# Performance work log

Hardware: AMD Instinct MI355X
Metric: run time of the kernel (lower is better)

The kernel has to match this reference:

```python
import jax, jax.numpy as jnp
import numpy as np

SELF_IMPORTANCE = 0.25  # blend weight for the node's own transformed features


def setup_inputs() -> dict:
    key = jax.random.key(0)
    k1, k2, k3, k4, k5 = jax.random.split(key, 5)
    F, newF, N = 128, 64, 500000
    return {
        "x": jax.random.normal(k1, (1, F), dtype=jnp.float32),
        "X": jax.random.normal(k2, (N, F), dtype=jnp.float32),
        "kernel": jax.random.normal(k3, (F, newF), dtype=jnp.float32) * (1.0 / np.sqrt(F)),
        "attn_self": jax.random.normal(k4, (newF, 1), dtype=jnp.float32) * (1.0 / np.sqrt(newF)),
        "attn_neigh": jax.random.normal(k5, (newF, 1), dtype=jnp.float32) * (1.0 / np.sqrt(newF)),
    }


def reference(x, X, kernel, attn_self, attn_neigh):
    # x: [1, F] node features; X: [N, F] neighbor features
    x_t = x @ kernel            # [1, newF]
    X_t = X @ kernel            # [N, newF]
    a_self = x_t @ attn_self    # [1, 1]
    a_neigh = X_t @ attn_neigh  # [N, 1]
    # repeat_elements(a_self, N) + a_neigh, then transpose -> [1, N]
    scores = (a_self + a_neigh).T
    # original adds mask = exp(-1e10) * -1e10 == -0.0 (a no-op); faithful softmax:
    attn = jax.nn.softmax(scores, axis=-1)  # [1, N]
    # Dropout is identity at inference (eval mode)
    feats_neigh = attn @ X_t    # [1, newF]
    return (1.0 - SELF_IMPORTANCE) * feats_neigh + SELF_IMPORTANCE * x_t
```

## Files before the change

kernel.cpp:

```cpp
#include <hip/hip_runtime.h>
#include <math.h>


#define TPB 256
#define MAXBLK 2048
#define PART_STRIDE 136
#define PART_BASE 256
#define FIN_TPB 512

__global__ __launch_bounds__(128) void gat_prep(
    const float* __restrict__ x, const float* __restrict__ kern,
    const float* __restrict__ attn_neigh, float* __restrict__ ws) {
  int t = threadIdx.x;
  float s = 0.f;
#pragma unroll 8
  for (int c = 0; c < 64; ++c) s += kern[t * 64 + c] * attn_neigh[c];
  ws[t] = s;
  if (t < 64) {
    float s2 = 0.f;
#pragma unroll 8
    for (int j = 0; j < 128; ++j) s2 += x[j] * kern[j * 64 + t];
    ws[128 + t] = s2;
  }
}

__global__ __launch_bounds__(TPB, 8) void gat_main(
    const float4* __restrict__ X4, const float* __restrict__ ws,
    float* __restrict__ part, int N, int totalWaves) {
  const int lane = threadIdx.x & 63;
  const int half = lane >> 5;
  const int hl = lane & 31;
  const int wid = threadIdx.x >> 6;
  const int gwave = blockIdx.x * (TPB / 64) + wid;

  const float4 wv = ((const float4*)ws)[hl];

  const int npairs = N >> 1;
  const int stride = totalWaves;

  float m = -INFINITY, l = 0.f;
  float ax = 0.f, ay = 0.f, az = 0.f, aw = 0.f;

  int p = gwave;
  float4 xv = make_float4(0.f, 0.f, 0.f, 0.f);
  if (p < npairs) xv = X4[(size_t)p * 64 + lane];

  for (; p + stride < npairs; p += stride) {
    const float4 xn = X4[(size_t)(p + stride) * 64 + lane];

    float s = xv.x * wv.x + xv.y * wv.y + xv.z * wv.z + xv.w * wv.w;
    s += __shfl_xor(s, 1);  s += __shfl_xor(s, 2);  s += __shfl_xor(s, 4);
    s += __shfl_xor(s, 8);  s += __shfl_xor(s, 16);
    const float mn = fmaxf(m, s);
    const float corr = __expf(m - mn);
    const float pw = __expf(s - mn);
    l = l * corr + pw;
    ax = ax * corr + pw * xv.x;  ay = ay * corr + pw * xv.y;
    az = az * corr + pw * xv.z;  aw = aw * corr + pw * xv.w;
    m = mn;

    xv = xn;
  }
  if (p < npairs) {
    float s = xv.x * wv.x + xv.y * wv.y + xv.z * wv.z + xv.w * wv.w;
    s += __shfl_xor(s, 1);  s += __shfl_xor(s, 2);  s += __shfl_xor(s, 4);
    s += __shfl_xor(s, 8);  s += __shfl_xor(s, 16);
    const float mn = fmaxf(m, s);
    const float corr = __expf(m - mn);
    const float pw = __expf(s - mn);
    l = l * corr + pw;
    ax = ax * corr + pw * xv.x;  ay = ay * corr + pw * xv.y;
    az = az * corr + pw * xv.z;  aw = aw * corr + pw * xv.w;
    m = mn;
  }

  if ((N & 1) && gwave == 0) {
    float4 tv = make_float4(0.f, 0.f, 0.f, 0.f);
    if (half == 0) tv = X4[(size_t)(N - 1) * 32 + hl];
    float s = tv.x * wv.x + tv.y * wv.y + tv.z * wv.z + tv.w * wv.w;
    s += __shfl_xor(s, 1);  s += __shfl_xor(s, 2);  s += __shfl_xor(s, 4);
    s += __shfl_xor(s, 8);  s += __shfl_xor(s, 16);
    if (half == 0) {
      const float mn = fmaxf(m, s);
      const float corr = __expf(m - mn);
      const float pw = __expf(s - mn);
      l = l * corr + pw;
      ax = ax * corr + pw * tv.x;  ay = ay * corr + pw * tv.y;
      az = az * corr + pw * tv.z;  aw = aw * corr + pw * tv.w;
      m = mn;
    }
  }

  const float m_o = __shfl_xor(m, 32);
  const float l_o = __shfl_xor(l, 32);
  const float axo = __shfl_xor(ax, 32);
  const float ayo = __shfl_xor(ay, 32);
  const float azo = __shfl_xor(az, 32);
  const float awo = __shfl_xor(aw, 32);
  const float M2 = fmaxf(m, m_o);
  const float c0 = (m == -INFINITY) ? 0.f : __expf(m - M2);
  const float c1 = (m_o == -INFINITY) ? 0.f : __expf(m_o - M2);
  const float l2 = l * c0 + l_o * c1;
  const float bx = ax * c0 + axo * c1;
  const float by = ay * c0 + ayo * c1;
  const float bz = az * c0 + azo * c1;
  const float bw = aw * c0 + awo * c1;

  __shared__ float sm[TPB / 64];
  __shared__ float sl[TPB / 64];
  __shared__ float sacc[TPB / 64][128];
  if (lane < 32) {
    sacc[wid][hl * 4 + 0] = bx;
    sacc[wid][hl * 4 + 1] = by;
    sacc[wid][hl * 4 + 2] = bz;
    sacc[wid][hl * 4 + 3] = bw;
    if (hl == 0) { sm[wid] = M2; sl[wid] = l2; }
  }
  __syncthreads();

  if (threadIdx.x < 32) {
    float Mb = -INFINITY;
#pragma unroll
    for (int w2 = 0; w2 < TPB / 64; ++w2) Mb = fmaxf(Mb, sm[w2]);
    float Lb = 0.f, fx = 0.f, fy = 0.f, fz = 0.f, fw = 0.f;
#pragma unroll
    for (int w2 = 0; w2 < TPB / 64; ++w2) {
      const float sc = (sm[w2] == -INFINITY) ? 0.f : __expf(sm[w2] - Mb);
      Lb += sc * sl[w2];
      fx += sc * sacc[w2][hl * 4 + 0];
      fy += sc * sacc[w2][hl * 4 + 1];
      fz += sc * sacc[w2][hl * 4 + 2];
      fw += sc * sacc[w2][hl * 4 + 3];
    }
    float* pb = part + (size_t)blockIdx.x * PART_STRIDE;
    if (hl == 0) { pb[0] = Mb; pb[1] = Lb; }
    float4 v = make_float4(fx, fy, fz, fw);
    ((float4*)(pb + 8))[hl] = v;
  }
}

__global__ __launch_bounds__(FIN_TPB) void gat_fin(
    const float* __restrict__ kern, const float* __restrict__ ws,
    float* __restrict__ out, int nblk) {
  __shared__ float scale[MAXBLK];
  __shared__ float red[FIN_TPB];
  __shared__ float fpart[4][128];
  __shared__ float feats[128];
  const int t = threadIdx.x;
  const float* part = ws + PART_BASE;

  float m = -INFINITY;
  for (int b = t; b < nblk; b += FIN_TPB) m = fmaxf(m, part[(size_t)b * PART_STRIDE]);
  red[t] = m;
  __syncthreads();
  for (int s = FIN_TPB / 2; s > 0; s >>= 1) {
    if (t < s) red[t] = fmaxf(red[t], red[t + s]);
    __syncthreads();
  }
  const float M = red[0];
  __syncthreads();

  float lp = 0.f;
  for (int b = t; b < nblk; b += FIN_TPB) {
    const float mb = part[(size_t)b * PART_STRIDE];
    const float sc = (mb == -INFINITY) ? 0.f : __expf(mb - M);
    scale[b] = sc;
    lp += sc * part[(size_t)b * PART_STRIDE + 1];
  }
  red[t] = lp;
  __syncthreads();
  for (int s = FIN_TPB / 2; s > 0; s >>= 1) {
    if (t < s) red[t] += red[t + s];
    __syncthreads();
  }
  const float L = red[0];
  __syncthreads();

  {
    const int j = t & 127;
    const int q = t >> 7;
    float f = 0.f;
    for (int b = q; b < nblk; b += 4) f += scale[b] * part[(size_t)b * PART_STRIDE + 8 + j];
    fpart[q][j] = f;
  }
  __syncthreads();
  if (t < 128) feats[t] = (fpart[0][t] + fpart[1][t] + fpart[2][t] + fpart[3][t]) / L;
  __syncthreads();

  if (t < 64) {
    float s = 0.f;
#pragma unroll 8
    for (int j = 0; j < 128; ++j) s += feats[j] * kern[j * 64 + t];
    out[t] = 0.75f * s + 0.25f * ws[128 + t];
  }
}

extern "C" void kernel_launch(void* const* d_in, const int* in_sizes, int n_in,
                              void* d_out, int out_size, void* d_ws, size_t ws_size,
                              hipStream_t stream) {
  const float* x          = (const float*)d_in[0];
  const float* X          = (const float*)d_in[1];
  const float* kern       = (const float*)d_in[2];
  const float* attn_neigh = (const float*)d_in[4];
  float* ws  = (float*)d_ws;
  float* out = (float*)d_out;

  const int N = in_sizes[1] / 128;

  int nblk = MAXBLK;
  const size_t availF = ws_size / 4;
  if (availF < (size_t)PART_BASE + (size_t)MAXBLK * PART_STRIDE) {
    long cap = ((long)availF - PART_BASE) / PART_STRIDE;
    nblk = (cap < 1) ? 1 : (int)cap;
  }
  const int totalWaves = nblk * (TPB / 64);

  gat_prep<<<1, 128, 0, stream>>>(x, kern, attn_neigh, ws);
  gat_main<<<nblk, TPB, 0, stream>>>((const float4*)X, ws, ws + PART_BASE,
                                     N, totalWaves);
  gat_fin<<<1, FIN_TPB, 0, stream>>>(kern, ws, out, nblk);
}
```

Measured before the change: 484.6 us.

## Deepen X prefetch, use fewer larger blocks, store partials column-major

The main kernel now keeps two rows of X loaded ahead instead of one. It launches 512 blocks of 512 threads instead of 2048 blocks of 256, which halves the total number of waves. Per-block softmax partials are stored column-major, so the final kernel reads them with unit stride and reduces each feature with wave shuffles. The aim is to keep memory-level parallelism with fewer blocks and to cheapen the finalize pass, at the risk of lower occupancy on a bandwidth-bound stream.

```diff
diff --git a/kernel.cpp b/kernel.cpp
--- a/kernel.cpp
+++ b/kernel.cpp
@@ -2,9 +2,8 @@
 #include <math.h>
 
 
-#define TPB 256
-#define MAXBLK 2048
-#define PART_STRIDE 136
+#define TPB 512
+#define NBLK 512
 #define PART_BASE 256
 #define FIN_TPB 512
 
@@ -24,55 +23,50 @@
   }
 }
 
-__global__ __launch_bounds__(TPB, 8) void gat_main(
+__global__ __launch_bounds__(TPB, 4) void gat_main(
     const float4* __restrict__ X4, const float* __restrict__ ws,
-    float* __restrict__ part, int N, int totalWaves) {
+    float* __restrict__ part, int N, int nblk) {
   const int lane = threadIdx.x & 63;
   const int half = lane >> 5;
   const int hl = lane & 31;
   const int wid = threadIdx.x >> 6;
   const int gwave = blockIdx.x * (TPB / 64) + wid;
+  const int stride = nblk * (TPB / 64);
 
   const float4 wv = ((const float4*)ws)[hl];
 
   const int npairs = N >> 1;
-  const int stride = totalWaves;
 
   float m = -INFINITY, l = 0.f;
   float ax = 0.f, ay = 0.f, az = 0.f, aw = 0.f;
 
+#define PROC(XV)                                                            \
+  {                                                                         \
+    float s = (XV).x * wv.x + (XV).y * wv.y + (XV).z * wv.z + (XV).w * wv.w;\
+    s += __shfl_xor(s, 1);  s += __shfl_xor(s, 2);  s += __shfl_xor(s, 4);  \
+    s += __shfl_xor(s, 8);  s += __shfl_xor(s, 16);                         \
+    const float mn = fmaxf(m, s);                                           \
+    const float corr = __expf(m - mn);               \
+    const float pw = __expf(s - mn);                                        \
+    l = l * corr + pw;                                                      \
+    ax = ax * corr + pw * (XV).x;  ay = ay * corr + pw * (XV).y;            \
+    az = az * corr + pw * (XV).z;  aw = aw * corr + pw * (XV).w;            \
+    m = mn;                                                                 \
+  }
+
   int p = gwave;
-  float4 xv = make_float4(0.f, 0.f, 0.f, 0.f);
-  if (p < npairs) xv = X4[(size_t)p * 64 + lane];
-
-  for (; p + stride < npairs; p += stride) {
-    const float4 xn = X4[(size_t)(p + stride) * 64 + lane];
-
-    float s = xv.x * wv.x + xv.y * wv.y + xv.z * wv.z + xv.w * wv.w;
-    s += __shfl_xor(s, 1);  s += __shfl_xor(s, 2);  s += __shfl_xor(s, 4);
-    s += __shfl_xor(s, 8);  s += __shfl_xor(s, 16);
-    const float mn = fmaxf(m, s);
-    const float corr = __expf(m - mn);
-    const float pw = __expf(s - mn);
-    l = l * corr + pw;
-    ax = ax * corr + pw * xv.x;  ay = ay * corr + pw * xv.y;
-    az = az * corr + pw * xv.z;  aw = aw * corr + pw * xv.w;
-    m = mn;
-
-    xv = xn;
-  }
-  if (p < npairs) {
-    float s = xv.x * wv.x + xv.y * wv.y + xv.z * wv.z + xv.w * wv.w;
-    s += __shfl_xor(s, 1);  s += __shfl_xor(s, 2);  s += __shfl_xor(s, 4);
-    s += __shfl_xor(s, 8);  s += __shfl_xor(s, 16);
-    const float mn = fmaxf(m, s);
-    const float corr = __expf(m - mn);
-    const float pw = __expf(s - mn);
-    l = l * corr + pw;
-    ax = ax * corr + pw * xv.x;  ay = ay * corr + pw * xv.y;
-    az = az * corr + pw * xv.z;  aw = aw * corr + pw * xv.w;
-    m = mn;
-  }
+  float4 x0 = make_float4(0.f, 0.f, 0.f, 0.f);
+  float4 x1 = make_float4(0.f, 0.f, 0.f, 0.f);
+  if (p < npairs) x0 = X4[(size_t)p * 64 + lane];
+  if (p + stride < npairs) x1 = X4[(size_t)(p + stride) * 64 + lane];
+  for (; p + 2 * stride < npairs; p += stride) {
+    const float4 xn = X4[(size_t)(p + 2 * stride) * 64 + lane];
+    PROC(x0);
+    x0 = x1;
+    x1 = xn;
+  }
+  if (p < npairs) PROC(x0);
+  if (p + stride < npairs) PROC(x1);
 
   if ((N & 1) && gwave == 0) {
     float4 tv = make_float4(0.f, 0.f, 0.f, 0.f);
@@ -90,6 +84,7 @@
       m = mn;
     }
   }
+#undef PROC
 
   const float m_o = __shfl_xor(m, 32);
   const float l_o = __shfl_xor(l, 32);
@@ -132,25 +127,33 @@
       fz += sc * sacc[w2][hl * 4 + 2];
       fw += sc * sacc[w2][hl * 4 + 3];
     }
-    float* pb = part + (size_t)blockIdx.x * PART_STRIDE;
-    if (hl == 0) { pb[0] = Mb; pb[1] = Lb; }
-    float4 v = make_float4(fx, fy, fz, fw);
-    ((float4*)(pb + 8))[hl] = v;
+    const int b = blockIdx.x;
+    float* part_m = part;
+    float* part_l = part + nblk;
+    float* part_a = part + 2 * nblk;
+    if (hl == 0) { part_m[b] = Mb; part_l[b] = Lb; }
+    part_a[(size_t)(4 * hl + 0) * nblk + b] = fx;
+    part_a[(size_t)(4 * hl + 1) * nblk + b] = fy;
+    part_a[(size_t)(4 * hl + 2) * nblk + b] = fz;
+    part_a[(size_t)(4 * hl + 3) * nblk + b] = fw;
   }
 }
 
 __global__ __launch_bounds__(FIN_TPB) void gat_fin(
     const float* __restrict__ kern, const float* __restrict__ ws,
     float* __restrict__ out, int nblk) {
-  __shared__ float scale[MAXBLK];
+  __shared__ float scale[NBLK];
   __shared__ float red[FIN_TPB];
-  __shared__ float fpart[4][128];
   __shared__ float feats[128];
   const int t = threadIdx.x;
-  const float* part = ws + PART_BASE;
+  const int lane = t & 63;
+  const int wid = t >> 6;
+  const float* part_m = ws + PART_BASE;
+  const float* part_l = part_m + nblk;
+  const float* part_a = part_l + nblk;
 
   float m = -INFINITY;
-  for (int b = t; b < nblk; b += FIN_TPB) m = fmaxf(m, part[(size_t)b * PART_STRIDE]);
+  for (int b = t; b < nblk; b += FIN_TPB) m = fmaxf(m, part_m[b]);
   red[t] = m;
   __syncthreads();
   for (int s = FIN_TPB / 2; s > 0; s >>= 1) {
@@ -162,10 +165,10 @@
 
   float lp = 0.f;
   for (int b = t; b < nblk; b += FIN_TPB) {
-    const float mb = part[(size_t)b * PART_STRIDE];
+    const float mb = part_m[b];
     const float sc = (mb == -INFINITY) ? 0.f : __expf(mb - M);
     scale[b] = sc;
-    lp += sc * part[(size_t)b * PART_STRIDE + 1];
+    lp += sc * part_l[b];
   }
   red[t] = lp;
   __syncthreads();
@@ -176,15 +179,14 @@
   const float L = red[0];
   __syncthreads();
 
-  {
-    const int j = t & 127;
-    const int q = t >> 7;
+  for (int jj = 0; jj < 16; ++jj) {
+    const int j = wid * 16 + jj;
     float f = 0.f;
-    for (int b = q; b < nblk; b += 4) f += scale[b] * part[(size_t)b * PART_STRIDE + 8 + j];
-    fpart[q][j] = f;
-  }
-  __syncthreads();
-  if (t < 128) feats[t] = (fpart[0][t] + fpart[1][t] + fpart[2][t] + fpart[3][t]) / L;
+    for (int b = lane; b < nblk; b += 64) f += scale[b] * part_a[(size_t)j * nblk + b];
+    f += __shfl_xor(f, 1);  f += __shfl_xor(f, 2);  f += __shfl_xor(f, 4);
+    f += __shfl_xor(f, 8);  f += __shfl_xor(f, 16); f += __shfl_xor(f, 32);
+    if (lane == 0) feats[j] = f / L;
+  }
   __syncthreads();
 
   if (t < 64) {
@@ -207,16 +209,15 @@
 
   const int N = in_sizes[1] / 128;
 
-  int nblk = MAXBLK;
+  int nblk = NBLK;
   const size_t availF = ws_size / 4;
-  if (availF < (size_t)PART_BASE + (size_t)MAXBLK * PART_STRIDE) {
-    long cap = ((long)availF - PART_BASE) / PART_STRIDE;
+  if (availF < (size_t)PART_BASE + (size_t)NBLK * 130) {
+    long cap = ((long)availF - PART_BASE) / 130;
     nblk = (cap < 1) ? 1 : (int)cap;
   }
-  const int totalWaves = nblk * (TPB / 64);
 
   gat_prep<<<1, 128, 0, stream>>>(x, kern, attn_neigh, ws);
   gat_main<<<nblk, TPB, 0, stream>>>((const float4*)X, ws, ws + PART_BASE,
-                                     N, totalWaves);
+                                     N, nblk);
   gat_fin<<<1, FIN_TPB, 0, stream>>>(kern, ws, out, nblk);
 }
```

Result: faster. 396.5 us (-18.2%).
